# Kernel optimization log

Measured on AMD Instinct MI355X. Metric: run time of the kernel, lower is better.

## Reference

```python
import jax, jax.numpy as jnp
import numpy as np


def _samx_row(qqq, kkk, vvv):
    """Suffix-automaton qkv retrieval over binary alphabet {0,1}.
    Faithful port of samx_qkv_slow, with dict transitions replaced by two
    flat transition arrays (alphabet size is 2 after the >0 binarization).
    """
    n = len(qqq)
    y = [0] * n
    s = 2 * n + 1
    tr = [[-1] * s, [-1] * s]   # tr[sym][state] = next state, -1 = absent
    f = [-1] * s                # suffix links
    m = [0] * s                 # max length of state
    r = [-1] * s                # last end position seen
    g = 0                       # last state
    u = 1                       # next free state id
    w = 0                       # current match state (query side)
    h = 0                       # current match length
    for i in range(n):
        q = qqq[i]
        k = kkk[i]
        tq = tr[q]
        tk = tr[k]
        # --- query: extend match with symbol q, following suffix links ---
        p, x = w, h
        while p != -1 and tq[p] == -1:
            if x > m[p]:
                x = m[p]
            p = f[p]
        if p != -1:
            p, x = tq[p], x + 1
        else:
            p, x = 0, 0
        # find tightest state for match length x
        vst = p
        while f[vst] != -1 and m[f[vst]] >= x:
            vst = f[vst]
        # back off to a state with positive length and a recorded endpos
        while vst != -1 and (m[vst] <= 0 or r[vst] < 0):
            vst = f[vst]
        yi = vvv[r[vst] + 1] if vst != -1 else -1
        y[i] = yi if yi > 0 else 0
        w, h = p, x
        # --- key: standard suffix-automaton extension with symbol k ---
        j = u
        u += 1
        m[j] = m[g] + 1
        p = g
        while p != -1 and tk[p] == -1:
            tk[p] = j
            p = f[p]
        if p == -1:
            f[j] = 0
        else:
            d = tk[p]
            if m[p] + 1 == m[d]:
                f[j] = d
            else:
                b = u
                u += 1
                tr[0][b] = tr[0][d]
                tr[1][b] = tr[1][d]
                m[b] = m[p] + 1
                f[b] = f[d]
                r[b] = r[d]
                f[d] = b
                f[j] = b
                while p != -1 and tk[p] == d:
                    tk[p] = b
                    p = f[p]
        # propagate latest end position up the suffix-link chain
        vst = g = j
        while vst != -1 and r[vst] < i:
            r[vst] = i
            vst = f[vst]
    return y


def _samx_idx(q, k, v):
    """q,k,v: float arrays [b,t,c] -> int idx [b,t,c] in {0,1}."""
    b, t, c = q.shape
    qb = (np.asarray(q) > 0).astype(np.uint8).transpose(0, 2, 1).reshape(-1, t)
    kb = (np.asarray(k) > 0).astype(np.uint8).transpose(0, 2, 1).reshape(-1, t)
    vb = (np.asarray(v) > 0).astype(np.uint8).transpose(0, 2, 1).reshape(-1, t)
    rows = [_samx_row(qq.tolist(), kk.tolist(), vv.tolist())
            for qq, kk, vv in zip(qb, kb, vb)]
    idx = np.asarray(rows, dtype=np.uint8).reshape(b, c, t).transpose(0, 2, 1)
    return idx


def setup_inputs() -> dict:
    key = jax.random.key(0)
    kq, kk, kv = jax.random.split(key, 3)
    B, T, C = 4, 2048, 256
    q = jax.random.normal(kq, (B, T, C), dtype=jnp.float32)
    k = jax.random.normal(kk, (B, T, C), dtype=jnp.float32)
    v = jax.random.normal(kv, (B, T, C), dtype=jnp.float32)
    e = jnp.ones((1, 1, C), dtype=jnp.float32)
    return {"q": q, "k": k, "v": v, "e": e}


def reference(q, k, v, e):
    # Irregular pointer-chasing part runs on host (numpy); output scaling in jnp.
    idx = _samx_idx(q, k, v)                      # [b,t,c] in {0,1}
    sign = 2.0 * jnp.asarray(idx, dtype=q.dtype) - 1.0
    return sign * e
```

## Files before the change

### kernel.cpp

```cpp
#include <hip/hip_runtime.h>


#define NSTATES 4096
#define TLEN 2048

typedef unsigned long long u64m;

__device__ __forceinline__ int f_tr(u64m r, int s) {
  return (int)(short)(unsigned short)(r >> (s << 4));
}
__device__ __forceinline__ int f_fl(u64m r) {
  return (int)(short)(unsigned short)(r >> 32);
}
__device__ __forceinline__ int f_ml(u64m r) {
  return (int)(r >> 48);
}
__device__ __forceinline__ u64m set_tr(u64m r, int s, int v) {
  const int sh = s << 4;
  return (r & ~(0xFFFFull << sh)) | ((u64m)(unsigned short)v << sh);
}

__device__ __forceinline__ int lane_shr1(int v, int lane) {
  int sh = __builtin_amdgcn_update_dpp(0, v, 0x111 , 0xF, 0xF, true);
  const int v15 = __builtin_amdgcn_readlane(v, 15);
  const int v31 = __builtin_amdgcn_readlane(v, 31);
  const int v47 = __builtin_amdgcn_readlane(v, 47);
  if (lane == 16) sh = v15;
  if (lane == 32) sh = v31;
  if (lane == 48) sh = v47;
  return sh;
}

__global__ __launch_bounds__(64)
void samx_main(const float* __restrict__ q,
               const float* __restrict__ k,
               unsigned* __restrict__ outpos,
               int T, int C) {
  __shared__ u64m           reca[NSTATES];
  __shared__ unsigned short rla[NSTATES];

  unsigned short* recw = (unsigned short*)reca;
  unsigned*       rech = (unsigned*)reca;

  const int row = blockIdx.x;
  const int b = row / C;
  const int c = row - b * C;
  const int lane = threadIdx.x;

  for (int s = lane; s < NSTATES; s += 64) {
    reca[s] = 0x0000FFFFFFFFFFFFull;
    rla[s] = 0xFFFFu;
  }

  const size_t rowbase = (size_t)b * (size_t)T * (size_t)C + (size_t)c;
  const float* qr = q + rowbase;
  const float* kr = k + rowbase;
  unsigned* outr = outpos + rowbase;

  unsigned qw = 0u, kw = 0u;
  {
    const int t0 = lane * 32;
#pragma unroll 8
    for (int jj = 0; jj < 32; ++jj) {
      const int t = t0 + jj;
      if (qr[(size_t)t * C] > 0.0f) qw |= (1u << jj);
      if (kr[(size_t)t * C] > 0.0f) kw |= (1u << jj);
    }
  }
  __syncthreads();

  int cid = 0;
  bool cval = (lane == 0);
  bool trunc = false;

  int g = 0;
  int mlg = 0;
  int u = 1;
  int w = 0;
  int h = 0;

  int qs = (int)(__builtin_amdgcn_readlane((int)qw, 0) & 1);
  int ks = (int)(__builtin_amdgcn_readlane((int)kw, 0) & 1);
  u64m pf_rec = reca[0];
  u64m recp   = pf_rec;

  for (int i = 0; i < T; ++i) {
    const bool hot = !trunc;
    const u64m rk  = pf_rec;
    const int img  = f_tr(rk, ks);
    const int myml = f_ml(rk);

    const int j = u++;
    const int mlj = mlg + 1;

    int d = -1, bb = -1, flj = 0, ndd = 0, newlen = 2, pushed = 0;
    bool prefl = false, inrun = false;

    if (hot) {
      const u64m brkmask = __ballot(cval && img != -1);
      const bool nobrk = (brkmask == 0);
      const int t2 = nobrk ? 64 : (int)__builtin_ctzll(brkmask);
      const int t2c = (t2 > 63) ? 63 : t2;
      d = __builtin_amdgcn_readlane(img, t2c);
      const int mlp = __builtin_amdgcn_readlane(myml, t2c);
      const int dld = (d < 0) ? 0 : d;
      prefl = cval && (lane < t2);

      const u64m recd = reca[dld];

      const int previmg = lane_shr1(img, lane);
      const bool rs = cval && lane >= t2 && (lane == t2 || img != previmg);
      const u64m rsmask = __ballot(rs);
      ndd = (int)__builtin_popcountll(rsmask);
      newlen = ndd + 2;
      const unsigned below =
          __builtin_amdgcn_mbcnt_hi((unsigned)(rsmask >> 32),
              __builtin_amdgcn_mbcnt_lo((unsigned)rsmask, 0u));
      const int dst = rs ? ((int)below + 1) : 0;
      pushed = __builtin_amdgcn_ds_permute(dst << 2, img);

      int dtr0 = f_tr(recd, 0);
      int dtr1 = f_tr(recd, 1);
      const unsigned fmdhi = (unsigned)(recd >> 32);
      if (!nobrk) {
        const int mld = (int)(fmdhi >> 16);
        if (mlp + 1 == mld) {
          flj = d;
        } else {
          bb = u++;
          const u64m pb = __ballot(prefl && cid == d);
          if (pb != 0ull) { if (ks) dtr1 = j; else dtr0 = j; }
          if (lane == 0) {
            reca[bb] = (u64m)(unsigned short)dtr0
                     | ((u64m)(unsigned short)dtr1 << 16)
                     | ((u64m)(fmdhi & 0xFFFFu) << 32)
                     | ((u64m)(unsigned)(mlp + 1) << 48);
          }
          flj = bb;
        }
      }
      if (lane == 0)
        rech[2 * j + 1] = (unsigned)(flj & 0xFFFF) | ((unsigned)mlj << 16);

      if (bb >= 0) {
        const u64m eq = __ballot(cval && img == d) >> t2;
        const int runlen = (eq == ~0ull) ? 64 : (int)__builtin_ctzll(~eq);
        inrun = cval && lane >= t2 && lane < t2 + runlen;
      }
    }

    int p = w, x = h;
    {
      u64m rr = recp;
      for (;;) {
        if (p == -1) { p = 0; x = 0; break; }
        const int tv = f_tr(rr, qs);
        if (tv != -1) { p = tv; x = x + 1; break; }
        const int mp = f_ml(rr);
        if (x > mp) x = mp;
        p = f_fl(rr);
        if (p == -1) { p = 0; x = 0; break; }
        rr = reca[p];
      }
    }

    const u64m recP = reca[p];
    int rlv = (int)(short)rla[p];
    unsigned fmv = (unsigned)(recP >> 32);
    int vst = p;
    for (;;) {
      const int fv = (int)(short)(fmv & 0xFFFFu);
      if (fv == -1) break;
      const unsigned fmf = rech[2 * fv + 1];
      const int rlf = (int)(short)rla[fv];
      if ((int)(fmf >> 16) < x) break;
      vst = fv; fmv = fmf; rlv = rlf;
    }
    int rv = -1;
    for (;;) {
      if (vst == -1) { rv = -1; break; }
      if ((int)(fmv >> 16) > 0 && rlv >= 0) { rv = rlv; break; }
      vst = (int)(short)(fmv & 0xFFFFu);
      if (vst == -1) { rv = -1; break; }
      fmv = rech[2 * vst + 1];
      rlv = (int)(short)rla[vst];
    }
    w = p; h = x;

    if (hot) {
      if (prefl) recw[4 * cid + ks] = (unsigned short)j;
      if (inrun) recw[4 * cid + ks] = (unsigned short)bb;
      if (bb >= 0 && lane == 0) recw[4 * d + 2] = (unsigned short)bb;
      if (lane == 0) outr[(size_t)i * C] = (unsigned)(rv + 1);

      u64m rp = recP;
      if (bb >= 0 && p == d)
        rp = (rp & ~(0xFFFFull << 32)) | ((u64m)(unsigned short)bb << 32);
      if (__ballot(prefl && cid == p) != 0ull) rp = set_tr(rp, ks, j);
      if (__ballot(inrun && cid == p) != 0ull) rp = set_tr(rp, ks, bb);
      recp = rp;

      int nv = 0;
      if (lane == 0) nv = j;
      else if (lane == 1) nv = flj;
      else if (lane - 1 < ndd) nv = pushed;
      const bool nval = (lane < newlen);
      if (nval) rla[nv] = (unsigned short)i;

      const bool overflow = (newlen > 64);
      if (overflow) {
        const int nv63 = __builtin_amdgcn_readlane(nv, 63);
        if (lane == 0) {
          int vp = (int)(short)(rech[2 * nv63 + 1] & 0xFFFFu);
          while (vp != -1) {
            rla[vp] = (unsigned short)i;
            vp = (int)(short)(rech[2 * vp + 1] & 0xFFFFu);
          }
        }
      }
      cid = nv; cval = nval; trunc = overflow;
    } else {
      int pcur = g, d2 = -1, idbrk = -1;
      for (;;) {
        if (pcur == -1) break;
        const u64m rr = reca[pcur];
        const int tv = f_tr(rr, ks);
        if (tv != -1) { d2 = tv; idbrk = pcur; break; }
        if (lane == 0) recw[4 * pcur + ks] = (unsigned short)j;
        pcur = f_fl(rr);
      }
      int fl2 = 0;
      if (d2 != -1) {
        const int mlp2 = f_ml(reca[idbrk]);
        const u64m rd2 = reca[d2];
        const int mld = f_ml(rd2);
        if (mlp2 + 1 == mld) {
          fl2 = d2;
        } else {
          const int bbc = u++;
          const int drl = (int)(short)rla[d2];
          if (lane == 0) {
            reca[bbc] = (u64m)(unsigned short)f_tr(rd2, 0)
                      | ((u64m)(unsigned short)f_tr(rd2, 1) << 16)
                      | ((u64m)((unsigned)(rd2 >> 32) & 0xFFFFu) << 32)
                      | ((u64m)(unsigned)(mlp2 + 1) << 48);
            rla[bbc] = (unsigned short)drl;
            recw[4 * d2 + 2] = (unsigned short)bbc;
          }
          fl2 = bbc;
          int p3 = idbrk;
          for (;;) {
            if (p3 == -1) break;
            const u64m r3 = reca[p3];
            const int tv3 = f_tr(r3, ks);
            if (tv3 != d2) break;
            if (lane == 0) recw[4 * p3 + ks] = (unsigned short)bbc;
            p3 = f_fl(r3);
          }
        }
      }
      if (lane == 0) {
        rech[2 * j + 1] = (unsigned)(fl2 & 0xFFFF) | ((unsigned)mlj << 16);
        outr[(size_t)i * C] = (unsigned)(rv + 1);
      }
      int vp = j, ncs = 0;
      bool tr2 = false;
      for (;;) {
        if (vp == -1) break;
        if (ncs < 64) { if (lane == ncs) cid = vp; ++ncs; }
        else tr2 = true;
        if (lane == 0) rla[vp] = (unsigned short)i;
        vp = (int)(short)(rech[2 * vp + 1] & 0xFFFFu);
      }
      cval = (lane < ncs);
      trunc = tr2;
      recp = reca[w];
    }
    g = j; mlg = mlj;

    if (i + 1 < T) {
      pf_rec = reca[cid];
      const int in = i + 1;
      const unsigned qwn = (unsigned)__builtin_amdgcn_readlane((int)qw, in >> 5);
      const unsigned kwn = (unsigned)__builtin_amdgcn_readlane((int)kw, in >> 5);
      qs = (int)((qwn >> (in & 31)) & 1u);
      ks = (int)((kwn >> (in & 31)) & 1u);
    }
  }
}

__global__ __launch_bounds__(256)
void samx_epilogue(const float* __restrict__ v,
                   const float* __restrict__ e,
                   unsigned* __restrict__ out,
                   int T, int C, int total) {
  const int idx = blockIdx.x * 256 + threadIdx.x;
  if (idx >= total) return;
  const unsigned vidx = out[idx];
  const int c = idx % C;
  const int bi = idx / C;
  const int b = bi / T;
  const float ev = e[c];
  float val = -ev;
  if (vidx != 0u) {
    if (v[((size_t)b * (size_t)T + (size_t)vidx) * (size_t)C + (size_t)c] > 0.0f)
      val = ev;
  }
  out[idx] = __float_as_uint(val);
}

extern "C" void kernel_launch(void* const* d_in, const int* in_sizes, int n_in,
                              void* d_out, int out_size, void* d_ws, size_t ws_size,
                              hipStream_t stream) {
  const float* q = (const float*)d_in[0];
  const float* k = (const float*)d_in[1];
  const float* v = (const float*)d_in[2];
  const float* e = (const float*)d_in[3];

  const int C = in_sizes[3];
  const int T = TLEN;
  const int B = in_sizes[0] / (T * C);
  const int total = out_size;

  samx_main<<<dim3(B * C), dim3(64), 0, stream>>>(q, k, (unsigned*)d_out, T, C);
  samx_epilogue<<<dim3((total + 255) / 256), dim3(256), 0, stream>>>(
      v, e, (unsigned*)d_out, T, C, total);
}
```

Measured before the change: 1.941 ms.

## Split key-side automaton update and query walk across two wavefronts

The block grows to two wavefronts. Wave 0 runs the key-side suffix-automaton extension while wave 1 runs the query match walk and the endpoint lookup. Two barriers per step order the read phase against the write phase. The aim is to overlap the two serial dependency chains that a single wave ran back to back. In exchange it adds two block barriers per step, gives up the prefetch and forwarded record (recp/pf_rec) trick, and doubles the threads per block, which may reduce how many blocks fit per CU.

```diff
diff --git a/kernel.cpp b/kernel.cpp
--- a/kernel.cpp
+++ b/kernel.cpp
@@ -14,10 +14,6 @@
 }
 __device__ __forceinline__ int f_ml(u64m r) {
   return (int)(r >> 48);
-}
-__device__ __forceinline__ u64m set_tr(u64m r, int s, int v) {
-  const int sh = s << 4;
-  return (r & ~(0xFFFFull << sh)) | ((u64m)(unsigned short)v << sh);
 }
 
 __device__ __forceinline__ int lane_shr1(int v, int lane) {
@@ -31,7 +27,7 @@
   return sh;
 }
 
-__global__ __launch_bounds__(64)
+__global__ __launch_bounds__(128)
 void samx_main(const float* __restrict__ q,
                const float* __restrict__ k,
                unsigned* __restrict__ outpos,
@@ -45,26 +41,24 @@
   const int row = blockIdx.x;
   const int b = row / C;
   const int c = row - b * C;
-  const int lane = threadIdx.x;
-
-  for (int s = lane; s < NSTATES; s += 64) {
+  const int lane = threadIdx.x & 63;
+  const int wid = threadIdx.x >> 6;
+
+  for (int s = threadIdx.x; s < NSTATES; s += 128) {
     reca[s] = 0x0000FFFFFFFFFFFFull;
     rla[s] = 0xFFFFu;
   }
 
   const size_t rowbase = (size_t)b * (size_t)T * (size_t)C + (size_t)c;
-  const float* qr = q + rowbase;
-  const float* kr = k + rowbase;
   unsigned* outr = outpos + rowbase;
 
-  unsigned qw = 0u, kw = 0u;
+  const float* src = (wid == 0 ? k : q) + rowbase;
+  unsigned bits = 0u;
   {
     const int t0 = lane * 32;
 #pragma unroll 8
     for (int jj = 0; jj < 32; ++jj) {
-      const int t = t0 + jj;
-      if (qr[(size_t)t * C] > 0.0f) qw |= (1u << jj);
-      if (kr[(size_t)t * C] > 0.0f) kw |= (1u << jj);
+      if (src[(size_t)(t0 + jj) * C] > 0.0f) bits |= (1u << jj);
     }
   }
   __syncthreads();
@@ -72,220 +66,214 @@
   int cid = 0;
   bool cval = (lane == 0);
   bool trunc = false;
-
   int g = 0;
   int mlg = 0;
   int u = 1;
   int w = 0;
   int h = 0;
 
-  int qs = (int)(__builtin_amdgcn_readlane((int)qw, 0) & 1);
-  int ks = (int)(__builtin_amdgcn_readlane((int)kw, 0) & 1);
-  u64m pf_rec = reca[0];
-  u64m recp   = pf_rec;
+  int sym = (int)(__builtin_amdgcn_readlane((int)bits, 0) & 1);
 
   for (int i = 0; i < T; ++i) {
     const bool hot = !trunc;
-    const u64m rk  = pf_rec;
-    const int img  = f_tr(rk, ks);
-    const int myml = f_ml(rk);
-
     const int j = u++;
     const int mlj = mlg + 1;
 
     int d = -1, bb = -1, flj = 0, ndd = 0, newlen = 2, pushed = 0;
     bool prefl = false, inrun = false;
 
-    if (hot) {
-      const u64m brkmask = __ballot(cval && img != -1);
-      const bool nobrk = (brkmask == 0);
-      const int t2 = nobrk ? 64 : (int)__builtin_ctzll(brkmask);
-      const int t2c = (t2 > 63) ? 63 : t2;
-      d = __builtin_amdgcn_readlane(img, t2c);
-      const int mlp = __builtin_amdgcn_readlane(myml, t2c);
-      const int dld = (d < 0) ? 0 : d;
-      prefl = cval && (lane < t2);
-
-      const u64m recd = reca[dld];
-
-      const int previmg = lane_shr1(img, lane);
-      const bool rs = cval && lane >= t2 && (lane == t2 || img != previmg);
-      const u64m rsmask = __ballot(rs);
-      ndd = (int)__builtin_popcountll(rsmask);
-      newlen = ndd + 2;
-      const unsigned below =
-          __builtin_amdgcn_mbcnt_hi((unsigned)(rsmask >> 32),
-              __builtin_amdgcn_mbcnt_lo((unsigned)rsmask, 0u));
-      const int dst = rs ? ((int)below + 1) : 0;
-      pushed = __builtin_amdgcn_ds_permute(dst << 2, img);
-
-      int dtr0 = f_tr(recd, 0);
-      int dtr1 = f_tr(recd, 1);
-      const unsigned fmdhi = (unsigned)(recd >> 32);
-      if (!nobrk) {
-        const int mld = (int)(fmdhi >> 16);
-        if (mlp + 1 == mld) {
-          flj = d;
-        } else {
-          bb = u++;
-          const u64m pb = __ballot(prefl && cid == d);
-          if (pb != 0ull) { if (ks) dtr1 = j; else dtr0 = j; }
+    if (wid == 0) {
+      if (hot) {
+        const int ks = sym;
+        const u64m rk = reca[cid];
+        const int img = f_tr(rk, ks);
+        const int myml = f_ml(rk);
+        const u64m brkmask = __ballot(cval && img != -1);
+        const bool nobrk = (brkmask == 0);
+        const int t2 = nobrk ? 64 : (int)__builtin_ctzll(brkmask);
+        const int t2c = (t2 > 63) ? 63 : t2;
+        d = __builtin_amdgcn_readlane(img, t2c);
+        const int mlp = __builtin_amdgcn_readlane(myml, t2c);
+        prefl = cval && (lane < t2);
+
+        const u64m recd = reca[d < 0 ? 0 : d];
+
+        const int previmg = lane_shr1(img, lane);
+        const bool rs = cval && lane >= t2 && (lane == t2 || img != previmg);
+        const u64m rsmask = __ballot(rs);
+        ndd = (int)__builtin_popcountll(rsmask);
+        newlen = ndd + 2;
+        const unsigned below =
+            __builtin_amdgcn_mbcnt_hi((unsigned)(rsmask >> 32),
+                __builtin_amdgcn_mbcnt_lo((unsigned)rsmask, 0u));
+        const int dst = rs ? ((int)below + 1) : 0;
+        pushed = __builtin_amdgcn_ds_permute(dst << 2, img);
+
+        int dtr0 = f_tr(recd, 0);
+        int dtr1 = f_tr(recd, 1);
+        const unsigned fmdhi = (unsigned)(recd >> 32);
+        if (!nobrk) {
+          const int mld = (int)(fmdhi >> 16);
+          if (mlp + 1 == mld) {
+            flj = d;
+          } else {
+            bb = u++;
+            const u64m pb = __ballot(prefl && cid == d);
+            if (pb != 0ull) { if (ks) dtr1 = j; else dtr0 = j; }
+            if (lane == 0) {
+              reca[bb] = (u64m)(unsigned short)dtr0
+                       | ((u64m)(unsigned short)dtr1 << 16)
+                       | ((u64m)(fmdhi & 0xFFFFu) << 32)
+                       | ((u64m)(unsigned)(mlp + 1) << 48);
+            }
+            flj = bb;
+          }
+        }
+        if (lane == 0)
+          rech[2 * j + 1] = (unsigned)(flj & 0xFFFF) | ((unsigned)mlj << 16);
+
+        if (bb >= 0) {
+          const u64m eq = __ballot(cval && img == d) >> t2;
+          const int runlen = (eq == ~0ull) ? 64 : (int)__builtin_ctzll(~eq);
+          inrun = cval && lane >= t2 && lane < t2 + runlen;
+        }
+      }
+    } else {
+      const int qs = sym;
+      int p = w, x = h;
+      {
+        u64m rr = reca[w];
+        for (;;) {
+          const int tv = f_tr(rr, qs);
+          if (tv != -1) { p = tv; x = x + 1; break; }
+          const int mp = f_ml(rr);
+          if (x > mp) x = mp;
+          p = f_fl(rr);
+          if (p == -1) { p = 0; x = 0; break; }
+          rr = reca[p];
+        }
+      }
+      const u64m recP = reca[p];
+      int rlv = (int)(short)rla[p];
+      unsigned fmv = (unsigned)(recP >> 32);
+      int vst = p;
+      for (;;) {
+        const int fv = (int)(short)(fmv & 0xFFFFu);
+        if (fv == -1) break;
+        const unsigned fmf = rech[2 * fv + 1];
+        const int rlf = (int)(short)rla[fv];
+        if ((int)(fmf >> 16) < x) break;
+        vst = fv; fmv = fmf; rlv = rlf;
+      }
+      int rv = -1;
+      for (;;) {
+        if (vst == -1) { rv = -1; break; }
+        if ((int)(fmv >> 16) > 0 && rlv >= 0) { rv = rlv; break; }
+        vst = (int)(short)(fmv & 0xFFFFu);
+        if (vst == -1) { rv = -1; break; }
+        fmv = rech[2 * vst + 1];
+        rlv = (int)(short)rla[vst];
+      }
+      w = p; h = x;
+      if (lane == 0) outr[(size_t)i * C] = (unsigned)(rv + 1);
+    }
+
+    asm volatile("" ::: "memory");
+    __builtin_amdgcn_s_barrier();
+    asm volatile("" ::: "memory");
+
+    if (wid == 0) {
+      const int ks = sym;
+      if (hot) {
+        if (prefl) recw[4 * cid + ks] = (unsigned short)j;
+        if (inrun) recw[4 * cid + ks] = (unsigned short)bb;
+        if (bb >= 0 && lane == 0) recw[4 * d + 2] = (unsigned short)bb;
+
+        int nv = 0;
+        if (lane == 0) nv = j;
+        else if (lane == 1) nv = flj;
+        else if (lane - 1 < ndd) nv = pushed;
+        const bool nval = (lane < newlen);
+        if (nval) rla[nv] = (unsigned short)i;
+
+        const bool overflow = (newlen > 64);
+        if (overflow) {
+          const int nv63 = __builtin_amdgcn_readlane(nv, 63);
           if (lane == 0) {
-            reca[bb] = (u64m)(unsigned short)dtr0
-                     | ((u64m)(unsigned short)dtr1 << 16)
-                     | ((u64m)(fmdhi & 0xFFFFu) << 32)
-                     | ((u64m)(unsigned)(mlp + 1) << 48);
+            int vp = (int)(short)(rech[2 * nv63 + 1] & 0xFFFFu);
+            while (vp != -1) {
+              rla[vp] = (unsigned short)i;
+              vp = (int)(short)(rech[2 * vp + 1] & 0xFFFFu);
+            }
           }
-          flj = bb;
-        }
-      }
-      if (lane == 0)
-        rech[2 * j + 1] = (unsigned)(flj & 0xFFFF) | ((unsigned)mlj << 16);
-
-      if (bb >= 0) {
-        const u64m eq = __ballot(cval && img == d) >> t2;
-        const int runlen = (eq == ~0ull) ? 64 : (int)__builtin_ctzll(~eq);
-        inrun = cval && lane >= t2 && lane < t2 + runlen;
-      }
+        }
+        cid = nv; cval = nval; trunc = overflow;
+      } else {
+        int pcur = g, d2 = -1, idbrk = -1;
+        for (;;) {
+          if (pcur == -1) break;
+          const u64m rr = reca[pcur];
+          const int tv = f_tr(rr, ks);
+          if (tv != -1) { d2 = tv; idbrk = pcur; break; }
+          if (lane == 0) recw[4 * pcur + ks] = (unsigned short)j;
+          pcur = f_fl(rr);
+        }
+        int fl2 = 0;
+        if (d2 != -1) {
+          const int mlp2 = f_ml(reca[idbrk]);
+          const u64m rd2 = reca[d2];
+          const int mld = f_ml(rd2);
+          if (mlp2 + 1 == mld) {
+            fl2 = d2;
+          } else {
+            const int bbc = u++;
+            const int drl = (int)(short)rla[d2];
+            if (lane == 0) {
+              reca[bbc] = (u64m)(unsigned short)f_tr(rd2, 0)
+                        | ((u64m)(unsigned short)f_tr(rd2, 1) << 16)
+                        | ((u64m)((unsigned)(rd2 >> 32) & 0xFFFFu) << 32)
+                        | ((u64m)(unsigned)(mlp2 + 1) << 48);
+              rla[bbc] = (unsigned short)drl;
+              recw[4 * d2 + 2] = (unsigned short)bbc;
+            }
+            fl2 = bbc;
+            int p3 = idbrk;
+            for (;;) {
+              if (p3 == -1) break;
+              const u64m r3 = reca[p3];
+              const int tv3 = f_tr(r3, ks);
+              if (tv3 != d2) break;
+              if (lane == 0) recw[4 * p3 + ks] = (unsigned short)bbc;
+              p3 = f_fl(r3);
+            }
+          }
+        }
+        if (lane == 0)
+          rech[2 * j + 1] = (unsigned)(fl2 & 0xFFFF) | ((unsigned)mlj << 16);
+        int vp = j, ncs = 0;
+        bool tr2 = false;
+        for (;;) {
+          if (vp == -1) break;
+          if (ncs < 64) { if (lane == ncs) cid = vp; ++ncs; }
+          else tr2 = true;
+          if (lane == 0) rla[vp] = (unsigned short)i;
+          vp = (int)(short)(rech[2 * vp + 1] & 0xFFFFu);
+        }
+        cval = (lane < ncs);
+        trunc = tr2;
+      }
+      g = j; mlg = mlj;
     }
 
-    int p = w, x = h;
-    {
-      u64m rr = recp;
-      for (;;) {
-        if (p == -1) { p = 0; x = 0; break; }
-        const int tv = f_tr(rr, qs);
-        if (tv != -1) { p = tv; x = x + 1; break; }
-        const int mp = f_ml(rr);
-        if (x > mp) x = mp;
-        p = f_fl(rr);
-        if (p == -1) { p = 0; x = 0; break; }
-        rr = reca[p];
-      }
+    if (i + 1 < T) {
+      const int in = i + 1;
+      const unsigned bw = (unsigned)__builtin_amdgcn_readlane((int)bits, in >> 5);
+      sym = (int)((bw >> (in & 31)) & 1u);
     }
 
-    const u64m recP = reca[p];
-    int rlv = (int)(short)rla[p];
-    unsigned fmv = (unsigned)(recP >> 32);
-    int vst = p;
-    for (;;) {
-      const int fv = (int)(short)(fmv & 0xFFFFu);
-      if (fv == -1) break;
-      const unsigned fmf = rech[2 * fv + 1];
-      const int rlf = (int)(short)rla[fv];
-      if ((int)(fmf >> 16) < x) break;
-      vst = fv; fmv = fmf; rlv = rlf;
-    }
-    int rv = -1;
-    for (;;) {
-      if (vst == -1) { rv = -1; break; }
-      if ((int)(fmv >> 16) > 0 && rlv >= 0) { rv = rlv; break; }
-      vst = (int)(short)(fmv & 0xFFFFu);
-      if (vst == -1) { rv = -1; break; }
-      fmv = rech[2 * vst + 1];
-      rlv = (int)(short)rla[vst];
-    }
-    w = p; h = x;
-
-    if (hot) {
-      if (prefl) recw[4 * cid + ks] = (unsigned short)j;
-      if (inrun) recw[4 * cid + ks] = (unsigned short)bb;
-      if (bb >= 0 && lane == 0) recw[4 * d + 2] = (unsigned short)bb;
-      if (lane == 0) outr[(size_t)i * C] = (unsigned)(rv + 1);
-
-      u64m rp = recP;
-      if (bb >= 0 && p == d)
-        rp = (rp & ~(0xFFFFull << 32)) | ((u64m)(unsigned short)bb << 32);
-      if (__ballot(prefl && cid == p) != 0ull) rp = set_tr(rp, ks, j);
-      if (__ballot(inrun && cid == p) != 0ull) rp = set_tr(rp, ks, bb);
-      recp = rp;
-
-      int nv = 0;
-      if (lane == 0) nv = j;
-      else if (lane == 1) nv = flj;
-      else if (lane - 1 < ndd) nv = pushed;
-      const bool nval = (lane < newlen);
-      if (nval) rla[nv] = (unsigned short)i;
-
-      const bool overflow = (newlen > 64);
-      if (overflow) {
-        const int nv63 = __builtin_amdgcn_readlane(nv, 63);
-        if (lane == 0) {
-          int vp = (int)(short)(rech[2 * nv63 + 1] & 0xFFFFu);
-          while (vp != -1) {
-            rla[vp] = (unsigned short)i;
-            vp = (int)(short)(rech[2 * vp + 1] & 0xFFFFu);
-          }
-        }
-      }
-      cid = nv; cval = nval; trunc = overflow;
-    } else {
-      int pcur = g, d2 = -1, idbrk = -1;
-      for (;;) {
-        if (pcur == -1) break;
-        const u64m rr = reca[pcur];
-        const int tv = f_tr(rr, ks);
-        if (tv != -1) { d2 = tv; idbrk = pcur; break; }
-        if (lane == 0) recw[4 * pcur + ks] = (unsigned short)j;
-        pcur = f_fl(rr);
-      }
-      int fl2 = 0;
-      if (d2 != -1) {
-        const int mlp2 = f_ml(reca[idbrk]);
-        const u64m rd2 = reca[d2];
-        const int mld = f_ml(rd2);
-        if (mlp2 + 1 == mld) {
-          fl2 = d2;
-        } else {
-          const int bbc = u++;
-          const int drl = (int)(short)rla[d2];
-          if (lane == 0) {
-            reca[bbc] = (u64m)(unsigned short)f_tr(rd2, 0)
-                      | ((u64m)(unsigned short)f_tr(rd2, 1) << 16)
-                      | ((u64m)((unsigned)(rd2 >> 32) & 0xFFFFu) << 32)
-                      | ((u64m)(unsigned)(mlp2 + 1) << 48);
-            rla[bbc] = (unsigned short)drl;
-            recw[4 * d2 + 2] = (unsigned short)bbc;
-          }
-          fl2 = bbc;
-          int p3 = idbrk;
-          for (;;) {
-            if (p3 == -1) break;
-            const u64m r3 = reca[p3];
-            const int tv3 = f_tr(r3, ks);
-            if (tv3 != d2) break;
-            if (lane == 0) recw[4 * p3 + ks] = (unsigned short)bbc;
-            p3 = f_fl(r3);
-          }
-        }
-      }
-      if (lane == 0) {
-        rech[2 * j + 1] = (unsigned)(fl2 & 0xFFFF) | ((unsigned)mlj << 16);
-        outr[(size_t)i * C] = (unsigned)(rv + 1);
-      }
-      int vp = j, ncs = 0;
-      bool tr2 = false;
-      for (;;) {
-        if (vp == -1) break;
-        if (ncs < 64) { if (lane == ncs) cid = vp; ++ncs; }
-        else tr2 = true;
-        if (lane == 0) rla[vp] = (unsigned short)i;
-        vp = (int)(short)(rech[2 * vp + 1] & 0xFFFFu);
-      }
-      cval = (lane < ncs);
-      trunc = tr2;
-      recp = reca[w];
-    }
-    g = j; mlg = mlj;
-
-    if (i + 1 < T) {
-      pf_rec = reca[cid];
-      const int in = i + 1;
-      const unsigned qwn = (unsigned)__builtin_amdgcn_readlane((int)qw, in >> 5);
-      const unsigned kwn = (unsigned)__builtin_amdgcn_readlane((int)kw, in >> 5);
-      qs = (int)((qwn >> (in & 31)) & 1u);
-      ks = (int)((kwn >> (in & 31)) & 1u);
-    }
+    asm volatile("s_waitcnt lgkmcnt(0)" ::: "memory");
+    __builtin_amdgcn_s_barrier();
+    asm volatile("" ::: "memory");
   }
 }
 
@@ -322,7 +310,7 @@
   const int B = in_sizes[0] / (T * C);
   const int total = out_size;
 
-  samx_main<<<dim3(B * C), dim3(64), 0, stream>>>(q, k, (unsigned*)d_out, T, C);
+  samx_main<<<dim3(B * C), dim3(128), 0, stream>>>(q, k, (unsigned*)d_out, T, C);
   samx_epilogue<<<dim3((total + 255) / 256), dim3(256), 0, stream>>>(
       v, e, (unsigned*)d_out, T, C, total);
 }
```

After: 1.577 ms. 18.7% less time.
